# Kernel tuning notes

Measured on AMD Instinct MI355X. Metric: run time of the kernel, lower is better.

The kernel has to match this reference:

```python
import jax, jax.numpy as jnp
import numpy as np

N = 50000   # nodes
D = 128     # feature / out_channels
E = 800000  # edges per edge type
L = 2       # num_layers
T = 2       # num edge types


def setup_inputs() -> dict:
    key = jax.random.key(0)
    ks = jax.random.split(key, 6)
    x = jax.random.normal(ks[0], (N, D), dtype=jnp.float32)
    h = jax.random.normal(ks[1], (N, D), dtype=jnp.float32)  # unused by forward, kept for fidelity
    edge_index_a = jax.random.randint(ks[2], (2, E), 0, N)
    edge_index_b = jax.random.randint(ks[3], (2, E), 0, N)
    Wl = (jax.random.normal(ks[4], (L, T, D, D), dtype=jnp.float32) * 0.05)
    bl = jnp.zeros((L, T, D), dtype=jnp.float32)
    Wr = (jax.random.normal(ks[5], (L, T, D, D), dtype=jnp.float32) * 0.05)
    return {"x": x, "h": h, "edge_index_a": edge_index_a, "edge_index_b": edge_index_b,
            "Wl": Wl, "bl": bl, "Wr": Wr}


def _sage(x, edge_index, Wl, bl, Wr):
    # PyG SAGEConv: lin_l(mean_{j->i} x_j) + lin_r(x_i); lin_l has bias, lin_r does not.
    src, dst = edge_index[0], edge_index[1]
    msg_sum = jax.ops.segment_sum(x[src], dst, num_segments=N)            # [N, D]
    deg = jax.ops.segment_sum(jnp.ones((edge_index.shape[1],), x.dtype), dst, num_segments=N)
    mean = msg_sum / jnp.maximum(deg, 1.0)[:, None]
    return mean @ Wl + bl + x @ Wr


def reference(x, h, edge_index_a, edge_index_b, Wl, bl, Wr):
    out = x
    for l in range(L):
        # HeteroConv default aggregation: sum over edge types with same dst node type
        out = (_sage(out, edge_index_a, Wl[l, 0], bl[l, 0], Wr[l, 0])
               + _sage(out, edge_index_b, Wl[l, 1], bl[l, 1], Wr[l, 1]))
    return jax.nn.sigmoid(out)
```

## Files before the change

### kernel.cpp

```cpp
#include <hip/hip_runtime.h>
#include <math.h>

#define N_NODES 50000
#define D 128
#define NE 800000
#define BN 64
#define NBUCK 782
#define CAP 1280
#define EPB 4096
#define PBLK 196
#define F2B_BLKS 6250
#define WPREP_BLKS 384
#define MPITCH 68

typedef unsigned int uint;
typedef unsigned short ushort;
typedef unsigned char uchar;

using bf16x8 = __attribute__((ext_vector_type(8))) short;
using f32x4  = __attribute__((ext_vector_type(4))) float;

__device__ __forceinline__ float bflo(uint w) {
    union { uint u; float f; } c; c.u = w << 16; return c.f;
}
__device__ __forceinline__ float bfhi(uint w) {
    union { uint u; float f; } c; c.u = w & 0xffff0000u; return c.f;
}
__device__ __forceinline__ uint fp2bf_rn(float f) {
    union { float f; uint u; } c; c.f = f;
    return (c.u + 0x7fffu + ((c.u >> 16) & 1u)) >> 16;
}

__global__ __launch_bounds__(256) void build_kernel(
    const float4* __restrict__ x4, uint2* __restrict__ featb2,
    uint* __restrict__ feat8w,
    const float* __restrict__ Wl, const float* __restrict__ Wr,
    ushort* __restrict__ Wpack,
    const int* __restrict__ srcA, const int* __restrict__ dstA,
    const int* __restrict__ srcB, const int* __restrict__ dstB,
    int* __restrict__ bcurA, int* __restrict__ bcurB,
    uint* __restrict__ ebufA, uint* __restrict__ ebufB) {
    const int blk = blockIdx.x;
    const int t   = threadIdx.x;
    if (blk < 2 * PBLK) {
        __shared__ int h[NBUCK];
        __shared__ int base[NBUCK];
        const int typ = blk >= PBLK;
        const int* src = typ ? srcB : srcA;
        const int* dst = typ ? dstB : dstA;
        int* bc        = typ ? bcurB : bcurA;
        uint* ebuf     = typ ? ebufB : ebufA;
        const int e0 = (blk - (typ ? PBLK : 0)) * EPB;
        for (int j = t; j < NBUCK; j += 256) h[j] = 0;
        __syncthreads();
#pragma unroll
        for (int i = 0; i < EPB / 256; ++i) {
            const int e = e0 + t + i * 256;
            if (e < NE) atomicAdd(&h[dst[e] >> 6], 1);
        }
        __syncthreads();
        for (int j = t; j < NBUCK; j += 256) {
            const int c = h[j];
            base[j] = c ? atomicAdd(&bc[j], c) : 0;
            h[j] = 0;
        }
        __syncthreads();
#pragma unroll
        for (int i = 0; i < EPB / 256; ++i) {
            const int e = e0 + t + i * 256;
            if (e < NE) {
                const int d  = dst[e];
                const int bk = d >> 6;
                const int pos = atomicAdd(&h[bk], 1);
                const int off = base[bk] + pos;
                if (off < CAP)
                    ebuf[(size_t)bk * CAP + off] = (uint)src[e] | ((uint)(d & 63) << 17);
            }
        }
    } else if (blk < 2 * PBLK + F2B_BLKS) {
        const int i = (blk - 2 * PBLK) * 256 + t;
        float4 v = x4[i];
        uint2 o;
        o.x = fp2bf_rn(v.x) | (fp2bf_rn(v.y) << 16);
        o.y = fp2bf_rn(v.z) | (fp2bf_rn(v.w) << 16);
        featb2[i] = o;
        int pk = __builtin_amdgcn_cvt_pk_fp8_f32(v.x, v.y, 0, false);
        pk = __builtin_amdgcn_cvt_pk_fp8_f32(v.z, v.w, pk, true);
        feat8w[i] = (uint)pk;
    } else {
        const int i   = (blk - 2 * PBLK - F2B_BLKS) * 256 + t;
        const int l   = i / 49152;
        const int rem = i % 49152;
        const int ks  = rem / 4096;
        const int n   = (rem % 4096) / 32;
        const int kk  = rem % 32;
        const int r   = ks * 32 + kk;
        float v;
        if (r < 128)       v = Wl[(((size_t)l * 2 + 0) * 128 + r) * 128 + n];
        else if (r < 256)  v = Wl[(((size_t)l * 2 + 1) * 128 + (r - 128)) * 128 + n];
        else               v = Wr[(((size_t)l * 2 + 0) * 128 + (r - 256)) * 128 + n]
                             + Wr[(((size_t)l * 2 + 1) * 128 + (r - 256)) * 128 + n];
        Wpack[i] = (ushort)fp2bf_rn(v);
    }
}

__global__ __launch_bounds__(1024, 8) void fused_kernel(
    const uint4* __restrict__ feat,
    const uint2* __restrict__ feat8,
    const uint* __restrict__ ebufA, const uint* __restrict__ ebufB,
    const int* __restrict__ bcntA, const int* __restrict__ bcntB,
    const ushort* __restrict__ Wpack,
    const float* __restrict__ bias0, const float* __restrict__ bias1,
    float* __restrict__ outf, ushort* __restrict__ outb,
    uchar* __restrict__ out8, int act) {

    __shared__ uint   mlds[2 * BN * MPITCH];
    __shared__ ushort lidx[2][CAP];
    __shared__ int    cnt[128], ex[128], cur[128];

    const int b = blockIdx.x;
    const int t = threadIdx.x;

    if (t < 128) cnt[t] = 0;
    __syncthreads();
    int countA = bcntA[b]; if (countA > CAP) countA = CAP;
    int countB = bcntB[b]; if (countB > CAP) countB = CAP;
    const uint* ebA = ebufA + (size_t)b * CAP;
    const uint* ebB = ebufB + (size_t)b * CAP;
    for (int e = t; e < countA; e += 1024) atomicAdd(&cnt[ebA[e] >> 17], 1);
    for (int e = t; e < countB; e += 1024) atomicAdd(&cnt[64 + (ebB[e] >> 17)], 1);
    __syncthreads();
    if (t < 128) ex[t] = cnt[t];
    __syncthreads();
    for (int off = 1; off < 64; off <<= 1) {
        int v = 0;
        if (t < 128 && (t & 63) >= off) v = ex[t - off];
        __syncthreads();
        if (t < 128 && (t & 63) >= off) ex[t] += v;
        __syncthreads();
    }
    if (t < 128) { ex[t] -= cnt[t]; cur[t] = ex[t]; }
    __syncthreads();
    for (int e = t; e < countA; e += 1024) {
        const uint rec = ebA[e];
        const int p = atomicAdd(&cur[rec >> 17], 1);
        lidx[0][p] = (ushort)(rec & 0x1FFFFu);
    }
    for (int e = t; e < countB; e += 1024) {
        const uint rec = ebB[e];
        const int p = atomicAdd(&cur[64 + (rec >> 17)], 1);
        lidx[1][p] = (ushort)(rec & 0x1FFFFu);
    }
    __syncthreads();

    const int cl = t >> 4, ln = t & 15;
#pragma unroll
    for (int typ = 0; typ < 2; ++typ) {
        const int beg = ex[typ * 64 + cl];
        const int fin = beg + cnt[typ * 64 + cl];
        const ushort* lx = lidx[typ];
        float a[8] = {0.f,0.f,0.f,0.f,0.f,0.f,0.f,0.f};
#define ACC8(w) { \
    auto p0 = __builtin_amdgcn_cvt_pk_f32_fp8((int)(w).x, false); \
    auto p1 = __builtin_amdgcn_cvt_pk_f32_fp8((int)(w).x, true);  \
    auto p2 = __builtin_amdgcn_cvt_pk_f32_fp8((int)(w).y, false); \
    auto p3 = __builtin_amdgcn_cvt_pk_f32_fp8((int)(w).y, true);  \
    a[0]+=p0[0]; a[1]+=p0[1]; a[2]+=p1[0]; a[3]+=p1[1];           \
    a[4]+=p2[0]; a[5]+=p2[1]; a[6]+=p3[0]; a[7]+=p3[1]; }
        int e = beg;
        for (; e + 4 <= fin; e += 4) {
            uint2 w0 = feat8[(size_t)lx[e]     * 16 + ln];
            uint2 w1 = feat8[(size_t)lx[e + 1] * 16 + ln];
            uint2 w2 = feat8[(size_t)lx[e + 2] * 16 + ln];
            uint2 w3 = feat8[(size_t)lx[e + 3] * 16 + ln];
            ACC8(w0); ACC8(w1); ACC8(w2); ACC8(w3);
        }
        for (; e < fin; ++e) {
            uint2 w0 = feat8[(size_t)lx[e] * 16 + ln];
            ACC8(w0);
        }
#undef ACC8
        const float invd = 1.0f / fmaxf((float)(fin - beg), 1.0f);
        uint4 o;
        o.x = fp2bf_rn(a[0] * invd) | (fp2bf_rn(a[1] * invd) << 16);
        o.y = fp2bf_rn(a[2] * invd) | (fp2bf_rn(a[3] * invd) << 16);
        o.z = fp2bf_rn(a[4] * invd) | (fp2bf_rn(a[5] * invd) << 16);
        o.w = fp2bf_rn(a[6] * invd) | (fp2bf_rn(a[7] * invd) << 16);
        *reinterpret_cast<uint4*>(&mlds[(typ * BN + cl) * MPITCH + ln * 4]) = o;
    }
    __syncthreads();

    const int wid = t >> 6, wl = t & 63;
    const int mrow = wl & 15, g = wl >> 4;
    const int mt   = wid >> 2;
    const int ntp  = (wid & 3) * 2;
    const int arow = mt * 16 + mrow;

    f32x4 acc0 = (f32x4){0.f, 0.f, 0.f, 0.f};
    f32x4 acc1 = (f32x4){0.f, 0.f, 0.f, 0.f};
#pragma unroll
    for (int ks = 0; ks < 12; ++ks) {
        union { uint4 u; bf16x8 v; } av;
        if (ks < 8) {
            av.u = *reinterpret_cast<const uint4*>(
                &mlds[((ks >> 2) * BN + arow) * MPITCH + (ks & 3) * 16 + g * 4]);
        } else {
            int srow = b * BN + arow;
            if (srow >= N_NODES) srow = N_NODES - 1;
            av.u = feat[(size_t)srow * 16 + (ks & 3) * 4 + g];
        }
        const ushort* Wk = Wpack + (size_t)ks * 128 * 32;
        union { uint4 u; bf16x8 v; } bv0, bv1;
        bv0.u = *reinterpret_cast<const uint4*>(Wk + ((ntp * 16 + mrow) * 32 + g * 8));
        bv1.u = *reinterpret_cast<const uint4*>(Wk + (((ntp + 1) * 16 + mrow) * 32 + g * 8));
        acc0 = __builtin_amdgcn_mfma_f32_16x16x32_bf16(av.v, bv0.v, acc0, 0, 0, 0);
        acc1 = __builtin_amdgcn_mfma_f32_16x16x32_bf16(av.v, bv1.v, acc1, 0, 0, 0);
    }

#pragma unroll
    for (int q = 0; q < 2; ++q) {
        const f32x4 av = q ? acc1 : acc0;
        const int col = (ntp + q) * 16 + mrow;
        const float bias = bias0[col] + bias1[col];
#pragma unroll
        for (int r = 0; r < 4; ++r) {
            const int row = b * BN + mt * 16 + g * 4 + r;
            if (row < N_NODES) {
                const float v = av[r] + bias;
                if (act) {
                    outf[(size_t)row * D + col] = 1.0f / (1.0f + expf(-v));
                } else {
                    outb[(size_t)row * D + col] = (ushort)fp2bf_rn(v);
                    const int pk = __builtin_amdgcn_cvt_pk_fp8_f32(v, v, 0, false);
                    out8[(size_t)row * D + col] = (uchar)(pk & 0xFF);
                }
            }
        }
    }
}

extern "C" void kernel_launch(void* const* d_in, const int* in_sizes, int n_in,
                              void* d_out, int out_size, void* d_ws, size_t ws_size,
                              hipStream_t stream) {
    const float* x    = (const float*)d_in[0];
    const int*   ei_a = (const int*)d_in[2];
    const int*   ei_b = (const int*)d_in[3];
    const float* Wl   = (const float*)d_in[4];
    const float* bl   = (const float*)d_in[5];
    const float* Wr   = (const float*)d_in[6];
    float* out = (float*)d_out;

    ushort* featb = (ushort*)d_ws;
    ushort* feat2 = featb + (size_t)N_NODES * D;
    uchar* feat8  = (uchar*)(feat2 + (size_t)N_NODES * D);
    uchar* feat28 = feat8 + (size_t)N_NODES * D;
    uint* ebufA = (uint*)(feat28 + (size_t)N_NODES * D);
    uint* ebufB = ebufA + (size_t)NBUCK * CAP;
    int* bcurA  = (int*)(ebufB + (size_t)NBUCK * CAP);
    int* bcurB  = bcurA + NBUCK;
    ushort* Wpack = (ushort*)(((size_t)(bcurB + NBUCK) + 63) & ~(size_t)63);

    const int* srcA = ei_a;
    const int* dstA = ei_a + NE;
    const int* srcB = ei_b;
    const int* dstB = ei_b + NE;

    hipMemsetAsync(bcurA, 0, 2ull * NBUCK * sizeof(int), stream);
    build_kernel<<<2 * PBLK + F2B_BLKS + WPREP_BLKS, 256, 0, stream>>>(
        (const float4*)x, (uint2*)featb, (uint*)feat8, Wl, Wr, Wpack,
        srcA, dstA, srcB, dstB, bcurA, bcurB, ebufA, ebufB);

    fused_kernel<<<NBUCK, 1024, 0, stream>>>(
        (const uint4*)featb, (const uint2*)feat8, ebufA, ebufB, bcurA, bcurB,
        Wpack, bl + 0 * D, bl + 1 * D, nullptr, feat2, feat28, 0);
    fused_kernel<<<NBUCK, 1024, 0, stream>>>(
        (const uint4*)feat2, (const uint2*)feat28, ebufA, ebufB, bcurA, bcurB,
        Wpack + (size_t)12 * 128 * 32, bl + 2 * D, bl + 3 * D, out, nullptr, nullptr, 1);
}
```

Measured before the change: 177.8 us.

## Stage edge records in LDS, balance gather by degree rank, unroll by 8

Edge records are copied once from global memory into LDS, so the counting and scatter passes no longer each read them from global. Nodes are ranked by in-degree per edge type, and the type-B pass walks that ranking in reverse. This pairs heavy and light nodes on the same 16-lane group across the two types to even out per-thread gather work. The gather loop is unrolled to 8 loads in flight. The cost is an extra 10KB of LDS per block, which may cut occupancy, plus a 64-step rank loop.

Measured after the change: 171.1 us, median of 3. -3.8%, faster.

```diff
diff --git a/kernel.cpp b/kernel.cpp
--- a/kernel.cpp
+++ b/kernel.cpp
@@ -115,20 +115,24 @@
     uchar* __restrict__ out8, int act) {
 
     __shared__ uint   mlds[2 * BN * MPITCH];
+    __shared__ uint   rlds[2][CAP];
     __shared__ ushort lidx[2][CAP];
     __shared__ int    cnt[128], ex[128], cur[128];
+    __shared__ uchar  rankedA[64], rankedB[64];
 
     const int b = blockIdx.x;
     const int t = threadIdx.x;
 
     if (t < 128) cnt[t] = 0;
-    __syncthreads();
     int countA = bcntA[b]; if (countA > CAP) countA = CAP;
     int countB = bcntB[b]; if (countB > CAP) countB = CAP;
     const uint* ebA = ebufA + (size_t)b * CAP;
     const uint* ebB = ebufB + (size_t)b * CAP;
-    for (int e = t; e < countA; e += 1024) atomicAdd(&cnt[ebA[e] >> 17], 1);
-    for (int e = t; e < countB; e += 1024) atomicAdd(&cnt[64 + (ebB[e] >> 17)], 1);
+    for (int e = t; e < countA; e += 1024) rlds[0][e] = ebA[e];
+    for (int e = t; e < countB; e += 1024) rlds[1][e] = ebB[e];
+    __syncthreads();
+    for (int e = t; e < countA; e += 1024) atomicAdd(&cnt[rlds[0][e] >> 17], 1);
+    for (int e = t; e < countB; e += 1024) atomicAdd(&cnt[64 + (rlds[1][e] >> 17)], 1);
     __syncthreads();
     if (t < 128) ex[t] = cnt[t];
     __syncthreads();
@@ -142,22 +146,37 @@
     if (t < 128) { ex[t] -= cnt[t]; cur[t] = ex[t]; }
     __syncthreads();
     for (int e = t; e < countA; e += 1024) {
-        const uint rec = ebA[e];
+        const uint rec = rlds[0][e];
         const int p = atomicAdd(&cur[rec >> 17], 1);
         lidx[0][p] = (ushort)(rec & 0x1FFFFu);
     }
     for (int e = t; e < countB; e += 1024) {
-        const uint rec = ebB[e];
+        const uint rec = rlds[1][e];
         const int p = atomicAdd(&cur[64 + (rec >> 17)], 1);
         lidx[1][p] = (ushort)(rec & 0x1FFFFu);
     }
+    if (t < 128) {
+        const int typ = t >> 6, i = t & 63;
+        const int li = cnt[t];
+        const int base = typ * 64;
+        int r = 0;
+#pragma unroll 8
+        for (int j = 0; j < 64; ++j) {
+            const int lj = cnt[base + j];
+            r += (lj > li) || (lj == li && j < i);
+        }
+        if (typ == 0) rankedA[r] = (uchar)i; else rankedB[r] = (uchar)i;
+    }
     __syncthreads();
 
     const int cl = t >> 4, ln = t & 15;
 #pragma unroll
     for (int typ = 0; typ < 2; ++typ) {
-        const int beg = ex[typ * 64 + cl];
-        const int fin = beg + cnt[typ * 64 + cl];
+        const int node = typ ? (int)rankedB[63 - cl] : (int)rankedA[cl];
+        const int slot = typ * 64 + node;
+        const int beg = ex[slot];
+        const int deg = cnt[slot];
+        const int fin = beg + deg;
         const ushort* lx = lidx[typ];
         float a[8] = {0.f,0.f,0.f,0.f,0.f,0.f,0.f,0.f};
 #define ACC8(w) { \
@@ -168,25 +187,38 @@
     a[0]+=p0[0]; a[1]+=p0[1]; a[2]+=p1[0]; a[3]+=p1[1];           \
     a[4]+=p2[0]; a[5]+=p2[1]; a[6]+=p3[0]; a[7]+=p3[1]; }
         int e = beg;
-        for (; e + 4 <= fin; e += 4) {
+        for (; e + 8 <= fin; e += 8) {
+            uint2 w0 = feat8[(size_t)lx[e]     * 16 + ln];
+            uint2 w1 = feat8[(size_t)lx[e + 1] * 16 + ln];
+            uint2 w2 = feat8[(size_t)lx[e + 2] * 16 + ln];
+            uint2 w3 = feat8[(size_t)lx[e + 3] * 16 + ln];
+            uint2 w4 = feat8[(size_t)lx[e + 4] * 16 + ln];
+            uint2 w5 = feat8[(size_t)lx[e + 5] * 16 + ln];
+            uint2 w6 = feat8[(size_t)lx[e + 6] * 16 + ln];
+            uint2 w7 = feat8[(size_t)lx[e + 7] * 16 + ln];
+            ACC8(w0); ACC8(w1); ACC8(w2); ACC8(w3);
+            ACC8(w4); ACC8(w5); ACC8(w6); ACC8(w7);
+        }
+        if (e + 4 <= fin) {
             uint2 w0 = feat8[(size_t)lx[e]     * 16 + ln];
             uint2 w1 = feat8[(size_t)lx[e + 1] * 16 + ln];
             uint2 w2 = feat8[(size_t)lx[e + 2] * 16 + ln];
             uint2 w3 = feat8[(size_t)lx[e + 3] * 16 + ln];
             ACC8(w0); ACC8(w1); ACC8(w2); ACC8(w3);
+            e += 4;
         }
         for (; e < fin; ++e) {
             uint2 w0 = feat8[(size_t)lx[e] * 16 + ln];
             ACC8(w0);
         }
 #undef ACC8
-        const float invd = 1.0f / fmaxf((float)(fin - beg), 1.0f);
+        const float invd = 1.0f / fmaxf((float)deg, 1.0f);
         uint4 o;
         o.x = fp2bf_rn(a[0] * invd) | (fp2bf_rn(a[1] * invd) << 16);
         o.y = fp2bf_rn(a[2] * invd) | (fp2bf_rn(a[3] * invd) << 16);
         o.z = fp2bf_rn(a[4] * invd) | (fp2bf_rn(a[5] * invd) << 16);
         o.w = fp2bf_rn(a[6] * invd) | (fp2bf_rn(a[7] * invd) << 16);
-        *reinterpret_cast<uint4*>(&mlds[(typ * BN + cl) * MPITCH + ln * 4]) = o;
+        *reinterpret_cast<uint4*>(&mlds[(typ * BN + node) * MPITCH + ln * 4]) = o;
     }
     __syncthreads();
 
```

## Precompute per-bucket CSR once and degree-sort gather work in fused kernel

Applied to the files above, without the earlier changes.

Adds a separate csrfill kernel that sorts each bucket's edge records into per-node CSR index lists once, along with per-node begin/degree arrays and a degree-descending ordering of the 128 (type,node) slots. Both layer kernels then skip the per-block LDS histogram, scan and scatter they previously each ran. The gather now uses 8 lanes per node with 16-byte fp8 loads and balances waves by processing heavy-degree nodes together. The cost is an extra kernel launch plus the global writes and reads of the index lists, and more registers for 16 accumulators.

Result: slower. 235.0 us (+32.2%).

```diff
diff --git a/kernel.cpp b/kernel.cpp
--- a/kernel.cpp
+++ b/kernel.cpp
@@ -104,89 +104,141 @@
     }
 }
 
+__global__ __launch_bounds__(256) void csrfill_kernel(
+    const uint* __restrict__ ebufA, const uint* __restrict__ ebufB,
+    const int* __restrict__ bcntA, const int* __restrict__ bcntB,
+    ushort* __restrict__ lidxA, ushort* __restrict__ lidxB,
+    int* __restrict__ pbeg, int* __restrict__ pdeg, uchar* __restrict__ ord) {
+    __shared__ uint rlds[2][CAP];
+    __shared__ int cnt[128], ex[128], cur[128];
+    const int b = blockIdx.x;
+    const int t = threadIdx.x;
+
+    if (t < 128) cnt[t] = 0;
+    int countA = bcntA[b]; if (countA > CAP) countA = CAP;
+    int countB = bcntB[b]; if (countB > CAP) countB = CAP;
+    const uint* ebA = ebufA + (size_t)b * CAP;
+    const uint* ebB = ebufB + (size_t)b * CAP;
+    for (int e = t; e < countA; e += 256) rlds[0][e] = ebA[e];
+    for (int e = t; e < countB; e += 256) rlds[1][e] = ebB[e];
+    __syncthreads();
+    for (int e = t; e < countA; e += 256) atomicAdd(&cnt[rlds[0][e] >> 17], 1);
+    for (int e = t; e < countB; e += 256) atomicAdd(&cnt[64 + (rlds[1][e] >> 17)], 1);
+    __syncthreads();
+    if (t < 128) ex[t] = cnt[t];
+    __syncthreads();
+    for (int off = 1; off < 64; off <<= 1) {
+        int v = 0;
+        if (t < 128 && (t & 63) >= off) v = ex[t - off];
+        __syncthreads();
+        if (t < 128 && (t & 63) >= off) ex[t] += v;
+        __syncthreads();
+    }
+    if (t < 128) {
+        ex[t] -= cnt[t];
+        cur[t] = ex[t];
+        const int node = b * BN + (t & 63);
+        if (node < N_NODES) {
+            const int base = (t >> 6) * N_NODES;
+            pbeg[base + node] = b * CAP + ex[t];
+            pdeg[base + node] = cnt[t];
+        }
+        const int li = cnt[t];
+        int r = 0;
+#pragma unroll 8
+        for (int j = 0; j < 128; ++j) {
+            const int lj = cnt[j];
+            r += (lj > li) || (lj == li && j < t);
+        }
+        ord[b * 128 + r] = (uchar)t;
+    }
+    __syncthreads();
+    for (int e = t; e < countA; e += 256) {
+        const uint rec = rlds[0][e];
+        const int p = atomicAdd(&cur[rec >> 17], 1);
+        lidxA[(size_t)b * CAP + p] = (ushort)(rec & 0x1FFFFu);
+    }
+    for (int e = t; e < countB; e += 256) {
+        const uint rec = rlds[1][e];
+        const int p = atomicAdd(&cur[64 + (rec >> 17)], 1);
+        lidxB[(size_t)b * CAP + p] = (ushort)(rec & 0x1FFFFu);
+    }
+}
+
 __global__ __launch_bounds__(1024, 8) void fused_kernel(
     const uint4* __restrict__ feat,
-    const uint2* __restrict__ feat8,
-    const uint* __restrict__ ebufA, const uint* __restrict__ ebufB,
-    const int* __restrict__ bcntA, const int* __restrict__ bcntB,
+    const uint4* __restrict__ feat8,
+    const ushort* __restrict__ lidxA, const ushort* __restrict__ lidxB,
+    const int* __restrict__ pbeg, const int* __restrict__ pdeg,
+    const uchar* __restrict__ ord,
     const ushort* __restrict__ Wpack,
     const float* __restrict__ bias0, const float* __restrict__ bias1,
     float* __restrict__ outf, ushort* __restrict__ outb,
     uchar* __restrict__ out8, int act) {
 
-    __shared__ uint   mlds[2 * BN * MPITCH];
-    __shared__ ushort lidx[2][CAP];
-    __shared__ int    cnt[128], ex[128], cur[128];
+    __shared__ uint  mlds[2 * BN * MPITCH];
+    __shared__ int   lbeg[128], ldeg[128];
+    __shared__ uchar lslot[128];
 
     const int b = blockIdx.x;
     const int t = threadIdx.x;
 
-    if (t < 128) cnt[t] = 0;
-    __syncthreads();
-    int countA = bcntA[b]; if (countA > CAP) countA = CAP;
-    int countB = bcntB[b]; if (countB > CAP) countB = CAP;
-    const uint* ebA = ebufA + (size_t)b * CAP;
-    const uint* ebB = ebufB + (size_t)b * CAP;
-    for (int e = t; e < countA; e += 1024) atomicAdd(&cnt[ebA[e] >> 17], 1);
-    for (int e = t; e < countB; e += 1024) atomicAdd(&cnt[64 + (ebB[e] >> 17)], 1);
-    __syncthreads();
-    if (t < 128) ex[t] = cnt[t];
-    __syncthreads();
-    for (int off = 1; off < 64; off <<= 1) {
-        int v = 0;
-        if (t < 128 && (t & 63) >= off) v = ex[t - off];
-        __syncthreads();
-        if (t < 128 && (t & 63) >= off) ex[t] += v;
-        __syncthreads();
-    }
-    if (t < 128) { ex[t] -= cnt[t]; cur[t] = ex[t]; }
-    __syncthreads();
-    for (int e = t; e < countA; e += 1024) {
-        const uint rec = ebA[e];
-        const int p = atomicAdd(&cur[rec >> 17], 1);
-        lidx[0][p] = (ushort)(rec & 0x1FFFFu);
-    }
-    for (int e = t; e < countB; e += 1024) {
-        const uint rec = ebB[e];
-        const int p = atomicAdd(&cur[64 + (rec >> 17)], 1);
-        lidx[1][p] = (ushort)(rec & 0x1FFFFu);
-    }
-    __syncthreads();
-
-    const int cl = t >> 4, ln = t & 15;
-#pragma unroll
-    for (int typ = 0; typ < 2; ++typ) {
-        const int beg = ex[typ * 64 + cl];
-        const int fin = beg + cnt[typ * 64 + cl];
-        const ushort* lx = lidx[typ];
-        float a[8] = {0.f,0.f,0.f,0.f,0.f,0.f,0.f,0.f};
-#define ACC8(w) { \
-    auto p0 = __builtin_amdgcn_cvt_pk_f32_fp8((int)(w).x, false); \
-    auto p1 = __builtin_amdgcn_cvt_pk_f32_fp8((int)(w).x, true);  \
-    auto p2 = __builtin_amdgcn_cvt_pk_f32_fp8((int)(w).y, false); \
-    auto p3 = __builtin_amdgcn_cvt_pk_f32_fp8((int)(w).y, true);  \
-    a[0]+=p0[0]; a[1]+=p0[1]; a[2]+=p1[0]; a[3]+=p1[1];           \
-    a[4]+=p2[0]; a[5]+=p2[1]; a[6]+=p3[0]; a[7]+=p3[1]; }
-        int e = beg;
-        for (; e + 4 <= fin; e += 4) {
-            uint2 w0 = feat8[(size_t)lx[e]     * 16 + ln];
-            uint2 w1 = feat8[(size_t)lx[e + 1] * 16 + ln];
-            uint2 w2 = feat8[(size_t)lx[e + 2] * 16 + ln];
-            uint2 w3 = feat8[(size_t)lx[e + 3] * 16 + ln];
-            ACC8(w0); ACC8(w1); ACC8(w2); ACC8(w3);
-        }
-        for (; e < fin; ++e) {
-            uint2 w0 = feat8[(size_t)lx[e] * 16 + ln];
-            ACC8(w0);
-        }
-#undef ACC8
-        const float invd = 1.0f / fmaxf((float)(fin - beg), 1.0f);
-        uint4 o;
-        o.x = fp2bf_rn(a[0] * invd) | (fp2bf_rn(a[1] * invd) << 16);
-        o.y = fp2bf_rn(a[2] * invd) | (fp2bf_rn(a[3] * invd) << 16);
-        o.z = fp2bf_rn(a[4] * invd) | (fp2bf_rn(a[5] * invd) << 16);
-        o.w = fp2bf_rn(a[6] * invd) | (fp2bf_rn(a[7] * invd) << 16);
-        *reinterpret_cast<uint4*>(&mlds[(typ * BN + cl) * MPITCH + ln * 4]) = o;
+    if (t < 128) {
+        const int slot = (int)ord[b * 128 + t];
+        lslot[t] = (uchar)slot;
+        const int node = b * BN + (slot & 63);
+        int bg = 0, dg = 0;
+        if (node < N_NODES) {
+            const int base = (slot >> 6) * N_NODES;
+            bg = pbeg[base + node];
+            dg = pdeg[base + node];
+        }
+        lbeg[t] = bg; ldeg[t] = dg;
+    }
+    __syncthreads();
+
+    const int j = t >> 3, ln = t & 7;
+    {
+        const int slot = (int)lslot[j];
+        const int typ = slot >> 6, lnode = slot & 63;
+        const int beg = lbeg[j], deg = ldeg[j];
+        const ushort* lx = (typ ? lidxB : lidxA) + beg;
+        float a[16] = {0.f,0.f,0.f,0.f,0.f,0.f,0.f,0.f,
+                       0.f,0.f,0.f,0.f,0.f,0.f,0.f,0.f};
+#define ACC16(vv) { \
+    auto q0 = __builtin_amdgcn_cvt_pk_f32_fp8((int)(vv).x, false); \
+    auto q1 = __builtin_amdgcn_cvt_pk_f32_fp8((int)(vv).x, true);  \
+    auto q2 = __builtin_amdgcn_cvt_pk_f32_fp8((int)(vv).y, false); \
+    auto q3 = __builtin_amdgcn_cvt_pk_f32_fp8((int)(vv).y, true);  \
+    auto q4 = __builtin_amdgcn_cvt_pk_f32_fp8((int)(vv).z, false); \
+    auto q5 = __builtin_amdgcn_cvt_pk_f32_fp8((int)(vv).z, true);  \
+    auto q6 = __builtin_amdgcn_cvt_pk_f32_fp8((int)(vv).w, false); \
+    auto q7 = __builtin_amdgcn_cvt_pk_f32_fp8((int)(vv).w, true);  \
+    a[0]+=q0[0];  a[1]+=q0[1];  a[2]+=q1[0];  a[3]+=q1[1];        \
+    a[4]+=q2[0];  a[5]+=q2[1];  a[6]+=q3[0];  a[7]+=q3[1];        \
+    a[8]+=q4[0];  a[9]+=q4[1];  a[10]+=q5[0]; a[11]+=q5[1];       \
+    a[12]+=q6[0]; a[13]+=q6[1]; a[14]+=q7[0]; a[15]+=q7[1]; }
+        int e = 0;
+        for (; e + 4 <= deg; e += 4) {
+            uint4 w0 = feat8[(size_t)lx[e]     * 8 + ln];
+            uint4 w1 = feat8[(size_t)lx[e + 1] * 8 + ln];
+            uint4 w2 = feat8[(size_t)lx[e + 2] * 8 + ln];
+            uint4 w3 = feat8[(size_t)lx[e + 3] * 8 + ln];
+            ACC16(w0); ACC16(w1); ACC16(w2); ACC16(w3);
+        }
+        for (; e < deg; ++e) {
+            uint4 w0 = feat8[(size_t)lx[e] * 8 + ln];
+            ACC16(w0);
+        }
+#undef ACC16
+        const float invd = 1.0f / fmaxf((float)deg, 1.0f);
+        uint o[8];
+#pragma unroll
+        for (int k = 0; k < 8; ++k)
+            o[k] = fp2bf_rn(a[2 * k] * invd) | (fp2bf_rn(a[2 * k + 1] * invd) << 16);
+        uint4* mp = reinterpret_cast<uint4*>(&mlds[(typ * BN + lnode) * MPITCH + ln * 8]);
+        mp[0] = make_uint4(o[0], o[1], o[2], o[3]);
+        mp[1] = make_uint4(o[4], o[5], o[6], o[7]);
     }
     __syncthreads();
 
@@ -256,8 +308,13 @@
     uchar* feat28 = feat8 + (size_t)N_NODES * D;
     uint* ebufA = (uint*)(feat28 + (size_t)N_NODES * D);
     uint* ebufB = ebufA + (size_t)NBUCK * CAP;
-    int* bcurA  = (int*)(ebufB + (size_t)NBUCK * CAP);
-    int* bcurB  = bcurA + NBUCK;
+    ushort* lidxA = (ushort*)(ebufB + (size_t)NBUCK * CAP);
+    ushort* lidxB = lidxA + (size_t)NBUCK * CAP;
+    int* pbeg  = (int*)(lidxB + (size_t)NBUCK * CAP);
+    int* pdeg  = pbeg + 2 * N_NODES;
+    uchar* ord = (uchar*)(pdeg + 2 * N_NODES);
+    int* bcurA = (int*)(((size_t)(ord + NBUCK * 128) + 15) & ~(size_t)15);
+    int* bcurB = bcurA + NBUCK;
     ushort* Wpack = (ushort*)(((size_t)(bcurB + NBUCK) + 63) & ~(size_t)63);
 
     const int* srcA = ei_a;
@@ -269,11 +326,13 @@
     build_kernel<<<2 * PBLK + F2B_BLKS + WPREP_BLKS, 256, 0, stream>>>(
         (const float4*)x, (uint2*)featb, (uint*)feat8, Wl, Wr, Wpack,
         srcA, dstA, srcB, dstB, bcurA, bcurB, ebufA, ebufB);
+    csrfill_kernel<<<NBUCK, 256, 0, stream>>>(
+        ebufA, ebufB, bcurA, bcurB, lidxA, lidxB, pbeg, pdeg, ord);
 
     fused_kernel<<<NBUCK, 1024, 0, stream>>>(
-        (const uint4*)featb, (const uint2*)feat8, ebufA, ebufB, bcurA, bcurB,
+        (const uint4*)featb, (const uint4*)feat8, lidxA, lidxB, pbeg, pdeg, ord,
         Wpack, bl + 0 * D, bl + 1 * D, nullptr, feat2, feat28, 0);
     fused_kernel<<<NBUCK, 1024, 0, stream>>>(
-        (const uint4*)feat2, (const uint2*)feat28, ebufA, ebufB, bcurA, bcurB,
+        (const uint4*)feat2, (const uint4*)feat28, lidxA, lidxB, pbeg, pdeg, ord,
         Wpack + (size_t)12 * 128 * 32, bl + 2 * D, bl + 3 * D, out, nullptr, nullptr, 1);
 }
```
